# Performance work log

Measured on AMD Instinct MI355X. Metric: run time of the kernel, lower is better.

## Reference

```python
import jax, jax.numpy as jnp
import numpy as np

EMBED_DIM = 1024
NUM_HEADS = 16
HEAD_DIM = EMBED_DIM // NUM_HEADS
B, N = 4, 2048
EPS = 1e-5


def rotate_half(x):
    x2d = x.reshape(x.shape[:-1] + (-1, 2))
    x1, x2 = x2d[..., 0], x2d[..., 1]
    return jnp.stack([-x2, x1], axis=-1).reshape(x.shape)


def apply_rotary_emb(freqs, t):
    return t * freqs[0] + rotate_half(t) * freqs[1]


def setup_inputs() -> dict:
    key = jax.random.key(0)
    ks = jax.random.split(key, 12)
    d = EMBED_DIM
    inp = {
        "x": jax.random.normal(ks[0], (B, N, d), jnp.float32),
        "encoding": jax.random.normal(ks[1], (2, N, HEAD_DIM), jnp.float32),
        "Wqkv_w": jax.random.normal(ks[2], (d, 3 * d), jnp.float32) * (1.0 / np.sqrt(d)),
        "Wqkv_b": jnp.zeros((3 * d,), jnp.float32),
        "out_w": jax.random.normal(ks[3], (d, d), jnp.float32) * (1.0 / np.sqrt(d)),
        "out_b": jnp.zeros((d,), jnp.float32),
        "ffn0_w": jax.random.normal(ks[4], (2 * d, 2 * d), jnp.float32) * (1.0 / np.sqrt(2 * d)),
        "ffn0_b": jnp.zeros((2 * d,), jnp.float32),
        "ln_scale": jnp.ones((2 * d,), jnp.float32),
        "ln_bias": jnp.zeros((2 * d,), jnp.float32),
        "ffn3_w": jax.random.normal(ks[5], (2 * d, d), jnp.float32) * (1.0 / np.sqrt(2 * d)),
        "ffn3_b": jnp.zeros((d,), jnp.float32),
    }
    return inp


def reference(x, encoding, Wqkv_w, Wqkv_b, out_w, out_b, ffn0_w, ffn0_b, ln_scale, ln_bias, ffn3_w, ffn3_b):
    b, n, d = x.shape
    # fused QKV projection
    qkv = jnp.einsum('bnd,de->bne', x, Wqkv_w) + Wqkv_b
    qkv = qkv.reshape(b, n, NUM_HEADS, HEAD_DIM, 3).transpose(0, 2, 1, 3, 4)  # (b,h,n,hd,3)
    q, k, v = qkv[..., 0], qkv[..., 1], qkv[..., 2]
    # RoPE (encoding broadcasts over batch/heads)
    q = apply_rotary_emb(encoding, q)
    k = apply_rotary_emb(encoding, k)
    # attention (no mask)
    scale = 1.0 / jnp.sqrt(jnp.asarray(HEAD_DIM, x.dtype))
    logits = jnp.einsum('bhqd,bhkd->bhqk', q, k) * scale
    attn = jax.nn.softmax(logits, axis=-1)
    context = jnp.einsum('bhqk,bhkd->bhqd', attn, v)
    message = context.transpose(0, 2, 1, 3).reshape(b, n, d)
    message = jnp.einsum('bnd,de->bne', message, out_w) + out_b
    # FFN: concat -> Dense -> LayerNorm -> GELU(exact) -> Dense
    h = jnp.concatenate([x, message], axis=-1)
    h = jnp.einsum('bnd,de->bne', h, ffn0_w) + ffn0_b
    mu = jnp.mean(h, axis=-1, keepdims=True)
    var = jnp.mean(jnp.square(h - mu), axis=-1, keepdims=True)
    h = (h - mu) * jax.lax.rsqrt(var + EPS) * ln_scale + ln_bias
    h = jax.nn.gelu(h, approximate=False)
    res = jnp.einsum('bnd,de->bne', h, ffn3_w) + ffn3_b
    return x + res
```

## Files before the change

### kernel.cpp

```cpp
#include <hip/hip_runtime.h>
#include <hip/hip_bf16.h>
#include <math.h>

typedef __bf16 bf16x8 __attribute__((ext_vector_type(8)));
typedef float f32x4 __attribute__((ext_vector_type(4)));

#define MFMA16(a, b, c) __builtin_amdgcn_mfma_f32_16x16x32_bf16((a), (b), (c), 0, 0, 0)

__device__ __forceinline__ void gload16(const void* g, void* l) {
  __builtin_amdgcn_global_load_lds((const __attribute__((address_space(1))) void*)g,
                                   (__attribute__((address_space(3))) void*)l, 16, 0, 0);
}

__global__ __launch_bounds__(256) void transpose_bf16(const float* __restrict__ in,
                                                      __bf16* __restrict__ out,
                                                      int K, int Nn) {
  __shared__ float tile[32][33];
  int n0 = blockIdx.x * 32, k0 = blockIdx.y * 32;
  int tx = threadIdx.x & 31, ty = threadIdx.x >> 5;
#pragma unroll
  for (int r = 0; r < 32; r += 8)
    tile[ty + r][tx] = in[(size_t)(k0 + ty + r) * Nn + n0 + tx];
  __syncthreads();
#pragma unroll
  for (int r = 0; r < 32; r += 8)
    out[(size_t)(n0 + ty + r) * K + k0 + tx] = (__bf16)tile[tx][ty + r];
}

__global__ __launch_bounds__(256) void convert_x(const float* __restrict__ x,
                                                 __bf16* __restrict__ h) {
  int id = blockIdx.x * 256 + threadIdx.x;
  int row = id >> 7, cc = id & 127;
  const float* src = x + (size_t)row * 1024 + cc * 8;
  __bf16 tmp[8];
#pragma unroll
  for (int e = 0; e < 8; ++e) tmp[e] = (__bf16)src[e];
  *(uint4*)(h + (size_t)row * 2048 + cc * 8) = *(uint4*)tmp;
}

template <typename OutT, bool HAS_RES>
__global__ __launch_bounds__(256) void gemm_kernel(
    const __bf16* __restrict__ A, int lda,
    const __bf16* __restrict__ Bt,
    const float* __restrict__ bias,
    OutT* __restrict__ C, int ldc,
    const float* __restrict__ res,
    int M, int Nn, int K) {
  __shared__ __attribute__((aligned(16))) __bf16 As[128 * 64];
  __shared__ __attribute__((aligned(16))) __bf16 Bs[128 * 64];

  const int t = threadIdx.x;
  const int row0A = blockIdx.x * 128;
  const int row0B = blockIdx.y * 128;
  const int wave = t >> 6, lane = t & 63;
  const int wm = wave >> 1, wn = wave & 1;
  const int g = lane >> 4, lr = lane & 15;

  f32x4 acc[4][4] = {};

  for (int k0 = 0; k0 < K; k0 += 64) {
#pragma unroll
    for (int p = 0; p < 4; ++p) {
      int cbase = (wave * 4 + p) * 64;
      int ci = cbase + lane;
      int r = ci >> 3, cp = ci & 7, cl = cp ^ (r & 7);
      gload16(A + (size_t)(row0A + r) * lda + k0 + cl * 8, &As[cbase * 8]);
      gload16(Bt + (size_t)(row0B + r) * K + k0 + cl * 8, &Bs[cbase * 8]);
    }
    __syncthreads();
#pragma unroll
    for (int kk = 0; kk < 2; ++kk) {
      bf16x8 af[4], bfr[4];
#pragma unroll
      for (int mt = 0; mt < 4; ++mt) {
        int r = wm * 64 + mt * 16 + lr, c = kk * 4 + g;
        af[mt] = *(const bf16x8*)((char*)As + r * 128 + ((c ^ (r & 7)) * 16));
      }
#pragma unroll
      for (int nt = 0; nt < 4; ++nt) {
        int r = wn * 64 + nt * 16 + lr, c = kk * 4 + g;
        bfr[nt] = *(const bf16x8*)((char*)Bs + r * 128 + ((c ^ (r & 7)) * 16));
      }
#pragma unroll
      for (int mt = 0; mt < 4; ++mt)
#pragma unroll
        for (int nt = 0; nt < 4; ++nt)
          acc[mt][nt] = MFMA16(af[mt], bfr[nt], acc[mt][nt]);
    }
    __syncthreads();
  }

  float bias_v[4];
#pragma unroll
  for (int nt = 0; nt < 4; ++nt) bias_v[nt] = bias[row0B + wn * 64 + nt * 16 + lr];
#pragma unroll
  for (int mt = 0; mt < 4; ++mt) {
    int grow_base = row0A + wm * 64 + mt * 16 + g * 4;
#pragma unroll
    for (int nt = 0; nt < 4; ++nt) {
      int gcol = row0B + wn * 64 + nt * 16 + lr;
#pragma unroll
      for (int j = 0; j < 4; ++j) {
        int grow = grow_base + j;
        float v = acc[mt][nt][j] + bias_v[nt];
        if (HAS_RES) v += res[(size_t)grow * ldc + gcol];
        C[(size_t)grow * ldc + gcol] = (OutT)v;
      }
    }
  }
}

__global__ __launch_bounds__(256) void rope_scatter(
    const __bf16* __restrict__ qkv, const float* __restrict__ enc,
    __bf16* __restrict__ q, __bf16* __restrict__ kk, __bf16* __restrict__ vt) {
  int bh = blockIdx.y;
  int b = bh >> 4, h = bh & 15;
  int n0 = blockIdx.x * 64;
  int t = threadIdx.x;
#pragma unroll
  for (int i = 0; i < 8; ++i) {
    int id = t + i * 256;
    int nl = id >> 5, p = id & 31;
    int n = n0 + nl;
    int d0 = 2 * p, d1 = 2 * p + 1;
    size_t base = ((size_t)(b * 2048 + n)) * 3072 + (h * 64 + d0) * 3;
    float q0 = (float)qkv[base + 0], k0 = (float)qkv[base + 1];
    float q1 = (float)qkv[base + 3], k1 = (float)qkv[base + 4];
    const float* e0 = enc + (size_t)n * 64;
    const float* e1 = enc + (size_t)131072 + (size_t)n * 64;
    float f00 = e0[d0], f01 = e0[d1], f10 = e1[d0], f11 = e1[d1];
    float qo0 = q0 * f00 - q1 * f10;
    float qo1 = q1 * f01 + q0 * f11;
    float ko0 = k0 * f00 - k1 * f10;
    float ko1 = k1 * f01 + k0 * f11;
    size_t qb = ((size_t)bh * 2048 + n) * 64 + d0;
    q[qb] = (__bf16)(qo0 * 0.125f);
    q[qb + 1] = (__bf16)(qo1 * 0.125f);
    kk[qb] = (__bf16)ko0;
    kk[qb + 1] = (__bf16)ko1;
  }
#pragma unroll
  for (int i = 0; i < 2; ++i) {
    int id = t + i * 256;
    int hd = id >> 3, c = id & 7;
    __bf16 tmp[8];
#pragma unroll
    for (int e = 0; e < 8; ++e) {
      int kv = (c >> 2) * 32 + (e >> 2) * 16 + (c & 3) * 4 + (e & 3);
      int n = n0 + kv;
      tmp[e] = qkv[((size_t)(b * 2048 + n)) * 3072 + (h * 64 + hd) * 3 + 2];
    }
    *(uint4*)(vt + ((size_t)bh * 64 + hd) * 2048 + n0 + c * 8) = *(uint4*)tmp;
  }
}

__global__ __launch_bounds__(256) void attn_kernel(
    const __bf16* __restrict__ q, const __bf16* __restrict__ k,
    const __bf16* __restrict__ vt, __bf16* __restrict__ ctx) {
  __shared__ __attribute__((aligned(16))) __bf16 Ks[2][64 * 64];
  __shared__ __attribute__((aligned(16))) __bf16 Vs[2][64 * 64];

  const int bh = blockIdx.y, b = bh >> 4, h = bh & 15;
  const int q0 = blockIdx.x * 64;
  const int t = threadIdx.x, wave = t >> 6, lane = t & 63;
  const int g = lane >> 4, lr = lane & 15;
  const int qrow = q0 + wave * 16;

  const __bf16* kbase = k + (size_t)bh * 2048 * 64;
  const __bf16* vbase = vt + (size_t)bh * 64 * 2048;

  bf16x8 qf[2];
#pragma unroll
  for (int kc = 0; kc < 2; ++kc)
    qf[kc] = *(const bf16x8*)(q + ((size_t)bh * 2048 + qrow + lr) * 64 + kc * 32 + g * 8);

  f32x4 o[4] = {};
  float lsum = 0.f;

#define STAGE_ATTN(buf, kv0)                                                    \
  {                                                                             \
    _Pragma("unroll") for (int p = 0; p < 2; ++p) {                             \
      int cbase = wave * 128 + p * 64;                                          \
      int ci = cbase + lane;                                                    \
      int r = ci >> 3, cp = ci & 7, cl = cp ^ (r & 7);                          \
      gload16(kbase + (size_t)((kv0) + r) * 64 + cl * 8, &Ks[buf][cbase * 8]);  \
      gload16(vbase + (size_t)r * 2048 + (kv0) + cl * 8, &Vs[buf][cbase * 8]);  \
    }                                                                           \
  }

  STAGE_ATTN(0, 0);
  __syncthreads();
  int buf = 0;

  for (int kv0 = 0; kv0 < 2048; kv0 += 64) {
    if (kv0 + 64 < 2048) STAGE_ATTN(buf ^ 1, kv0 + 64);

    f32x4 s[4];
#pragma unroll
    for (int nt = 0; nt < 4; ++nt) {
      int r = nt * 16 + lr;
      bf16x8 kf0 = *(const bf16x8*)((char*)Ks[buf] + r * 128 + (((0 * 4 + g) ^ (r & 7)) * 16));
      bf16x8 kf1 = *(const bf16x8*)((char*)Ks[buf] + r * 128 + (((1 * 4 + g) ^ (r & 7)) * 16));
      f32x4 a = {};
      a = MFMA16(kf0, qf[0], a);
      a = MFMA16(kf1, qf[1], a);
      s[nt] = a;
    }

    float pvv[4][4];
#pragma unroll
    for (int nt = 0; nt < 4; ++nt)
#pragma unroll
      for (int j = 0; j < 4; ++j) {
        float e = __expf(s[nt][j]);
        pvv[nt][j] = e;
        lsum += e;
      }

#pragma unroll
    for (int t2 = 0; t2 < 2; ++t2) {
      bf16x8 pf;
#pragma unroll
      for (int e = 0; e < 8; ++e) pf[e] = (__bf16)pvv[2 * t2 + (e >> 2)][e & 3];
#pragma unroll
      for (int nt = 0; nt < 4; ++nt) {
        int r = nt * 16 + lr;
        bf16x8 vf = *(const bf16x8*)((char*)Vs[buf] + r * 128 + (((t2 * 4 + g) ^ (r & 7)) * 16));
        o[nt] = MFMA16(vf, pf, o[nt]);
      }
    }
    __syncthreads();
    buf ^= 1;
  }

  lsum += __shfl_xor(lsum, 16, 64);
  lsum += __shfl_xor(lsum, 32, 64);
  float inv = 1.f / lsum;

  size_t obase = ((size_t)(b * 2048 + qrow + lr)) * 1024 + h * 64;
#pragma unroll
  for (int nt = 0; nt < 4; ++nt) {
    __bf16 w4[4];
#pragma unroll
    for (int j = 0; j < 4; ++j) w4[j] = (__bf16)(o[nt][j] * inv);
    *(uint2*)(ctx + obase + nt * 16 + g * 4) = *(uint2*)w4;
  }
#undef STAGE_ATTN
}

__global__ __launch_bounds__(256) void ln_gelu(const __bf16* __restrict__ hin,
                                               const float* __restrict__ lns,
                                               const float* __restrict__ lnb,
                                               __bf16* __restrict__ hout) {
  int row = blockIdx.x;
  const __bf16* rp = hin + (size_t)row * 2048;
  int t = threadIdx.x;
  __bf16 tmp[8];
  *(uint4*)tmp = *(const uint4*)(rp + t * 8);
  float vals[8], s = 0.f, s2 = 0.f;
#pragma unroll
  for (int e = 0; e < 8; ++e) {
    float x = (float)tmp[e];
    vals[e] = x;
    s += x;
    s2 += x * x;
  }
#pragma unroll
  for (int m = 1; m < 64; m <<= 1) {
    s += __shfl_xor(s, m, 64);
    s2 += __shfl_xor(s2, m, 64);
  }
  __shared__ float red[8];
  int wave = t >> 6, lane = t & 63;
  if (lane == 0) { red[wave] = s; red[4 + wave] = s2; }
  __syncthreads();
  s = red[0] + red[1] + red[2] + red[3];
  s2 = red[4] + red[5] + red[6] + red[7];
  float mu = s * (1.f / 2048.f);
  float var = s2 * (1.f / 2048.f) - mu * mu;
  float rstd = rsqrtf(var + 1e-5f);
  __bf16 outv[8];
#pragma unroll
  for (int e = 0; e < 8; ++e) {
    int c = t * 8 + e;
    float xh = (vals[e] - mu) * rstd * lns[c] + lnb[c];
    float gg = 0.5f * xh * (1.f + erff(xh * 0.70710678118f));
    outv[e] = (__bf16)gg;
  }
  *(uint4*)(hout + (size_t)row * 2048 + t * 8) = *(uint4*)outv;
}

extern "C" void kernel_launch(void* const* d_in, const int* in_sizes, int n_in,
                              void* d_out, int out_size, void* d_ws, size_t ws_size,
                              hipStream_t stream) {
  const float* x = (const float*)d_in[0];
  const float* enc = (const float*)d_in[1];
  const float* wqkv = (const float*)d_in[2];
  const float* bqkv = (const float*)d_in[3];
  const float* wout = (const float*)d_in[4];
  const float* bout = (const float*)d_in[5];
  const float* wffn0 = (const float*)d_in[6];
  const float* bffn0 = (const float*)d_in[7];
  const float* lns = (const float*)d_in[8];
  const float* lnb = (const float*)d_in[9];
  const float* wffn3 = (const float*)d_in[10];
  const float* bffn3 = (const float*)d_in[11];
  float* out = (float*)d_out;
  char* ws = (char*)d_ws;

  __bf16* wT_qkv = (__bf16*)(ws + 0);
  __bf16* wT_out = (__bf16*)(ws + 6291456);
  __bf16* wT_ffn0 = (__bf16*)(ws + 8388608);
  __bf16* wT_ffn3 = (__bf16*)(ws + 16777216);
  __bf16* h_in = (__bf16*)(ws + 20971520);
  __bf16* qkv = (__bf16*)(ws + 54525952);
  __bf16* ffn0o = qkv;
  __bf16* qb = (__bf16*)(ws + 104857600);
  __bf16* h2 = qb;
  __bf16* kb = (__bf16*)(ws + 121634816);
  __bf16* vtb = (__bf16*)(ws + 138412032);
  __bf16* ctx = (__bf16*)(ws + 155189248);

  dim3 blk(256);
  transpose_bf16<<<dim3(96, 32), blk, 0, stream>>>(wqkv, wT_qkv, 1024, 3072);
  transpose_bf16<<<dim3(32, 32), blk, 0, stream>>>(wout, wT_out, 1024, 1024);
  transpose_bf16<<<dim3(64, 64), blk, 0, stream>>>(wffn0, wT_ffn0, 2048, 2048);
  transpose_bf16<<<dim3(32, 64), blk, 0, stream>>>(wffn3, wT_ffn3, 2048, 1024);
  convert_x<<<4096, blk, 0, stream>>>(x, h_in);

  gemm_kernel<__bf16, false><<<dim3(64, 24), blk, 0, stream>>>(
      h_in, 2048, wT_qkv, bqkv, qkv, 3072, nullptr, 8192, 3072, 1024);

  rope_scatter<<<dim3(32, 64), blk, 0, stream>>>(qkv, enc, qb, kb, vtb);
  attn_kernel<<<dim3(32, 64), blk, 0, stream>>>(qb, kb, vtb, ctx);

  gemm_kernel<__bf16, false><<<dim3(64, 8), blk, 0, stream>>>(
      ctx, 1024, wT_out, bout, h_in + 1024, 2048, nullptr, 8192, 1024, 1024);

  gemm_kernel<__bf16, false><<<dim3(64, 16), blk, 0, stream>>>(
      h_in, 2048, wT_ffn0, bffn0, ffn0o, 2048, nullptr, 8192, 2048, 2048);

  ln_gelu<<<8192, blk, 0, stream>>>(ffn0o, lns, lnb, h2);

  gemm_kernel<float, true><<<dim3(64, 8), blk, 0, stream>>>(
      h2, 2048, wT_ffn3, bffn3, out, 1024, x, 8192, 1024, 2048);
}
```

Baseline: 422.9 us.

## Fold out-projection into FFN0 weights, add 256-tile pipelined GEMM, permute QKV layout

The out-projection weight is folded algebraically into the second half of the FFN0 weight, and its bias into the FFN0 bias. This removes the separate out-projection GEMM, and attention writes its context straight into the concat buffer. The QKV weight columns are permuted so that q, k and v come out contiguous, which lets the RoPE/scatter kernel use vectorized loads. A new 256x256 tile GEMM with a 4-stage global_load_lds pipeline, split barriers and setprio runs the QKV and FFN0 projections, and setprio hints are added around the attention MFMAs. The weight folding is recomputed every call, adding small prologue work, and it adds one more bf16 rounding step on the fused weights.

After: 467.1 us. 1.1x slower.

```diff
diff --git a/kernel.cpp b/kernel.cpp
--- a/kernel.cpp
+++ b/kernel.cpp
@@ -6,6 +6,7 @@
 typedef float f32x4 __attribute__((ext_vector_type(4)));
 
 #define MFMA16(a, b, c) __builtin_amdgcn_mfma_f32_16x16x32_bf16((a), (b), (c), 0, 0, 0)
+#define KAP(r) ((((r) + ((r) >> 2))) & 3)
 
 __device__ __forceinline__ void gload16(const void* g, void* l) {
   __builtin_amdgcn_global_load_lds((const __attribute__((address_space(1))) void*)g,
@@ -27,6 +28,43 @@
     out[(size_t)(n0 + ty + r) * K + k0 + tx] = (__bf16)tile[tx][ty + r];
 }
 
+__global__ __launch_bounds__(256) void transpose_qkv_perm(const float* __restrict__ in,
+                                                          __bf16* __restrict__ out) {
+  __shared__ float tile[32][33];
+  int n0 = blockIdx.x * 32, k0 = blockIdx.y * 32;
+  int tx = threadIdx.x & 31, ty = threadIdx.x >> 5;
+#pragma unroll
+  for (int r = 0; r < 32; r += 8)
+    tile[ty + r][tx] = in[(size_t)(k0 + ty + r) * 3072 + n0 + tx];
+  __syncthreads();
+#pragma unroll
+  for (int r = 0; r < 32; r += 8) {
+    int n = n0 + ty + r;
+    int h = n / 192, rem = n % 192, hd = rem / 3, which = rem % 3;
+    int np = which * 1024 + h * 64 + hd;
+    out[(size_t)np * 1024 + k0 + tx] = (__bf16)tile[tx][ty + r];
+  }
+}
+
+__global__ __launch_bounds__(256) void bias_perm(const float* __restrict__ b,
+                                                 float* __restrict__ bp) {
+  int n = blockIdx.x * 256 + threadIdx.x;
+  if (n < 3072) {
+    int h = n / 192, rem = n % 192, hd = rem / 3, which = rem % 3;
+    bp[which * 1024 + h * 64 + hd] = b[n];
+  }
+}
+
+__global__ __launch_bounds__(256) void convert_plain(const float* __restrict__ in,
+                                                     __bf16* __restrict__ out) {
+  int id = blockIdx.x * 256 + threadIdx.x;
+  const float* src = in + (size_t)id * 8;
+  __bf16 tmp[8];
+#pragma unroll
+  for (int e = 0; e < 8; ++e) tmp[e] = (__bf16)src[e];
+  *(uint4*)(out + (size_t)id * 8) = *(uint4*)tmp;
+}
+
 __global__ __launch_bounds__(256) void convert_x(const float* __restrict__ x,
                                                  __bf16* __restrict__ h) {
   int id = blockIdx.x * 256 + threadIdx.x;
@@ -38,7 +76,25 @@
   *(uint4*)(h + (size_t)row * 2048 + cc * 8) = *(uint4*)tmp;
 }
 
-template <typename OutT, bool HAS_RES>
+__global__ __launch_bounds__(256) void copy_cols(const __bf16* __restrict__ src,
+                                                 __bf16* __restrict__ dst) {
+  int id = blockIdx.x * 256 + threadIdx.x;
+  int row = id >> 7, c = id & 127;
+  *(uint4*)(dst + (size_t)row * 2048 + 1024 + c * 8) =
+      *(const uint4*)(src + (size_t)row * 1024 + c * 8);
+}
+
+__global__ __launch_bounds__(256) void fuse_bias(const float* __restrict__ bout,
+                                                 const float* __restrict__ w0,
+                                                 const float* __restrict__ b0,
+                                                 float* __restrict__ bf) {
+  int n = blockIdx.x * 256 + threadIdx.x;
+  float s = b0[n];
+  for (int e = 0; e < 1024; ++e) s += bout[e] * w0[(size_t)(1024 + e) * 2048 + n];
+  bf[n] = s;
+}
+
+template <typename OutT, bool HAS_RES, bool HAS_BIAS>
 __global__ __launch_bounds__(256) void gemm_kernel(
     const __bf16* __restrict__ A, int lda,
     const __bf16* __restrict__ Bt,
@@ -92,7 +148,8 @@
 
   float bias_v[4];
 #pragma unroll
-  for (int nt = 0; nt < 4; ++nt) bias_v[nt] = bias[row0B + wn * 64 + nt * 16 + lr];
+  for (int nt = 0; nt < 4; ++nt)
+    bias_v[nt] = HAS_BIAS ? bias[row0B + wn * 64 + nt * 16 + lr] : 0.f;
 #pragma unroll
   for (int mt = 0; mt < 4; ++mt) {
     int grow_base = row0A + wm * 64 + mt * 16 + g * 4;
@@ -106,6 +163,115 @@
         if (HAS_RES) v += res[(size_t)grow * ldc + gcol];
         C[(size_t)grow * ldc + gcol] = (OutT)v;
       }
+    }
+  }
+}
+
+template <typename OutT>
+__global__ __launch_bounds__(512, 2) void gemm256(
+    const __bf16* __restrict__ A, int lda,
+    const __bf16* __restrict__ Bt, int ldb,
+    const float* __restrict__ bias,
+    OutT* __restrict__ C, int ldc, int K) {
+  __shared__ __attribute__((aligned(16))) __bf16 lds[65536];
+  __bf16* Asl = lds;
+  __bf16* Bsl = lds + 32768;
+
+  const int t = threadIdx.x;
+  const int wave = t >> 6, lane = t & 63;
+  const int wm = wave >> 2, wn = wave & 3;
+  const int g = lane >> 4, lr = lane & 15;
+  const int row0A = blockIdx.x * 256, row0B = blockIdx.y * 256;
+
+  f32x4 acc[8][4] = {};
+  const int L = K >> 5;
+
+#define STAGE_A(s)                                                           \
+  {                                                                          \
+    int ssl = (s) & 3;                                                       \
+    _Pragma("unroll") for (int l = 0; l < 2; ++l) {                          \
+      int cbase = (wave * 2 + l) * 64;                                       \
+      int ci = cbase + lane, r = ci >> 2, c = (ci & 3) ^ KAP(r);             \
+      gload16(A + (size_t)(row0A + r) * lda + (s) * 32 + c * 8,              \
+              (void*)(Asl + ssl * 8192 + cbase * 8));                        \
+    }                                                                        \
+  }
+#define STAGE_B(s)                                                           \
+  {                                                                          \
+    int ssl = (s) & 3;                                                       \
+    _Pragma("unroll") for (int l = 0; l < 2; ++l) {                          \
+      int cbase = (wave * 2 + l) * 64;                                       \
+      int ci = cbase + lane, r = ci >> 2, c = (ci & 3) ^ KAP(r);             \
+      gload16(Bt + (size_t)(row0B + r) * ldb + (s) * 32 + c * 8,             \
+              (void*)(Bsl + ssl * 8192 + cbase * 8));                        \
+    }                                                                        \
+  }
+
+#define SLOT_BODY(s, DO_STAGE, VMSTR)                                        \
+  {                                                                          \
+    const __bf16* Ab = Asl + ((s) & 3) * 8192;                               \
+    const __bf16* Bb = Bsl + ((s) & 3) * 8192;                               \
+    bf16x8 bfrag[4], afrag[4];                                               \
+    _Pragma("unroll") for (int ni = 0; ni < 4; ++ni) {                       \
+      int rr = wn * 64 + ni * 16 + lr;                                       \
+      bfrag[ni] = *(const bf16x8*)(Bb + rr * 32 + ((g ^ KAP(rr)) * 8));      \
+    }                                                                        \
+    _Pragma("unroll") for (int mi = 0; mi < 4; ++mi) {                       \
+      int rr = wm * 128 + mi * 16 + lr;                                      \
+      afrag[mi] = *(const bf16x8*)(Ab + rr * 32 + ((g ^ KAP(rr)) * 8));      \
+    }                                                                        \
+    if (DO_STAGE) STAGE_A((s) + 3);                                          \
+    __builtin_amdgcn_s_barrier();                                            \
+    __builtin_amdgcn_s_setprio(1);                                           \
+    _Pragma("unroll") for (int mi = 0; mi < 4; ++mi)                         \
+      _Pragma("unroll") for (int ni = 0; ni < 4; ++ni)                       \
+        acc[mi][ni] = MFMA16(afrag[mi], bfrag[ni], acc[mi][ni]);             \
+    __builtin_amdgcn_s_setprio(0);                                           \
+    __builtin_amdgcn_s_barrier();                                            \
+    _Pragma("unroll") for (int mi = 0; mi < 4; ++mi) {                       \
+      int rr = wm * 128 + 64 + mi * 16 + lr;                                 \
+      afrag[mi] = *(const bf16x8*)(Ab + rr * 32 + ((g ^ KAP(rr)) * 8));      \
+    }                                                                        \
+    if (DO_STAGE) STAGE_B((s) + 3);                                          \
+    asm volatile("s_waitcnt " VMSTR ::: "memory");                           \
+    __builtin_amdgcn_s_barrier();                                            \
+    __builtin_amdgcn_s_setprio(1);                                           \
+    _Pragma("unroll") for (int mi = 0; mi < 4; ++mi)                         \
+      _Pragma("unroll") for (int ni = 0; ni < 4; ++ni)                       \
+        acc[4 + mi][ni] = MFMA16(afrag[mi], bfrag[ni], acc[4 + mi][ni]);     \
+    __builtin_amdgcn_s_setprio(0);                                           \
+    __builtin_amdgcn_s_barrier();                                            \
+  }
+
+#pragma unroll
+  for (int ss = 0; ss < 3; ++ss) {
+    STAGE_A(ss);
+    STAGE_B(ss);
+  }
+  asm volatile("s_waitcnt vmcnt(8)" ::: "memory");
+  __builtin_amdgcn_s_barrier();
+
+  for (int s = 0; s + 3 < L; ++s) SLOT_BODY(s, true, "vmcnt(8)");
+  SLOT_BODY(L - 3, false, "vmcnt(4)");
+  SLOT_BODY(L - 2, false, "vmcnt(0)");
+  SLOT_BODY(L - 1, false, "vmcnt(0)");
+
+#undef SLOT_BODY
+#undef STAGE_A
+#undef STAGE_B
+
+  float bias_v[4];
+#pragma unroll
+  for (int ni = 0; ni < 4; ++ni) bias_v[ni] = bias[row0B + wn * 64 + ni * 16 + lr];
+#pragma unroll
+  for (int mi = 0; mi < 8; ++mi) {
+    int grow_base = row0A + wm * 128 + mi * 16 + g * 4;
+#pragma unroll
+    for (int ni = 0; ni < 4; ++ni) {
+      int gcol = row0B + wn * 64 + ni * 16 + lr;
+#pragma unroll
+      for (int j = 0; j < 4; ++j)
+        C[(size_t)(grow_base + j) * ldc + gcol] = (OutT)(acc[mi][ni][j] + bias_v[ni]);
     }
   }
 }
@@ -118,26 +284,29 @@
   int n0 = blockIdx.x * 64;
   int t = threadIdx.x;
 #pragma unroll
-  for (int i = 0; i < 8; ++i) {
+  for (int i = 0; i < 2; ++i) {
     int id = t + i * 256;
-    int nl = id >> 5, p = id & 31;
+    int nl = id >> 3, cc = id & 7;
     int n = n0 + nl;
-    int d0 = 2 * p, d1 = 2 * p + 1;
-    size_t base = ((size_t)(b * 2048 + n)) * 3072 + (h * 64 + d0) * 3;
-    float q0 = (float)qkv[base + 0], k0 = (float)qkv[base + 1];
-    float q1 = (float)qkv[base + 3], k1 = (float)qkv[base + 4];
-    const float* e0 = enc + (size_t)n * 64;
-    const float* e1 = enc + (size_t)131072 + (size_t)n * 64;
-    float f00 = e0[d0], f01 = e0[d1], f10 = e1[d0], f11 = e1[d1];
-    float qo0 = q0 * f00 - q1 * f10;
-    float qo1 = q1 * f01 + q0 * f11;
-    float ko0 = k0 * f00 - k1 * f10;
-    float ko1 = k1 * f01 + k0 * f11;
-    size_t qb = ((size_t)bh * 2048 + n) * 64 + d0;
-    q[qb] = (__bf16)(qo0 * 0.125f);
-    q[qb + 1] = (__bf16)(qo1 * 0.125f);
-    kk[qb] = (__bf16)ko0;
-    kk[qb + 1] = (__bf16)ko1;
+    size_t row = (size_t)(b * 2048 + n) * 3072;
+    bf16x8 qv = *(const bf16x8*)(qkv + row + h * 64 + cc * 8);
+    bf16x8 kv = *(const bf16x8*)(qkv + row + 1024 + h * 64 + cc * 8);
+    const float* e0 = enc + (size_t)n * 64 + cc * 8;
+    const float* e1 = e0 + 131072;
+    __bf16 qo[8], ko[8];
+#pragma unroll
+    for (int e = 0; e < 8; e += 2) {
+      float q0 = (float)qv[e], q1 = (float)qv[e + 1];
+      float k0 = (float)kv[e], k1 = (float)kv[e + 1];
+      float f00 = e0[e], f01 = e0[e + 1], f10 = e1[e], f11 = e1[e + 1];
+      qo[e] = (__bf16)((q0 * f00 - q1 * f10) * 0.125f);
+      qo[e + 1] = (__bf16)((q1 * f01 + q0 * f11) * 0.125f);
+      ko[e] = (__bf16)(k0 * f00 - k1 * f10);
+      ko[e + 1] = (__bf16)(k1 * f01 + k0 * f11);
+    }
+    size_t qb = ((size_t)bh * 2048 + n) * 64 + cc * 8;
+    *(uint4*)(q + qb) = *(uint4*)qo;
+    *(uint4*)(kk + qb) = *(uint4*)ko;
   }
 #pragma unroll
   for (int i = 0; i < 2; ++i) {
@@ -148,7 +317,7 @@
     for (int e = 0; e < 8; ++e) {
       int kv = (c >> 2) * 32 + (e >> 2) * 16 + (c & 3) * 4 + (e & 3);
       int n = n0 + kv;
-      tmp[e] = qkv[((size_t)(b * 2048 + n)) * 3072 + (h * 64 + hd) * 3 + 2];
+      tmp[e] = qkv[(size_t)(b * 2048 + n) * 3072 + 2048 + h * 64 + hd];
     }
     *(uint4*)(vt + ((size_t)bh * 64 + hd) * 2048 + n0 + c * 8) = *(uint4*)tmp;
   }
@@ -196,16 +365,18 @@
     if (kv0 + 64 < 2048) STAGE_ATTN(buf ^ 1, kv0 + 64);
 
     f32x4 s[4];
+    __builtin_amdgcn_s_setprio(1);
 #pragma unroll
     for (int nt = 0; nt < 4; ++nt) {
       int r = nt * 16 + lr;
-      bf16x8 kf0 = *(const bf16x8*)((char*)Ks[buf] + r * 128 + (((0 * 4 + g) ^ (r & 7)) * 16));
-      bf16x8 kf1 = *(const bf16x8*)((char*)Ks[buf] + r * 128 + (((1 * 4 + g) ^ (r & 7)) * 16));
+      bf16x8 kf0 = *(const bf16x8*)((char*)Ks[buf] + r * 128 + ((g ^ (r & 7)) * 16));
+      bf16x8 kf1 = *(const bf16x8*)((char*)Ks[buf] + r * 128 + (((4 + g) ^ (r & 7)) * 16));
       f32x4 a = {};
       a = MFMA16(kf0, qf[0], a);
       a = MFMA16(kf1, qf[1], a);
       s[nt] = a;
     }
+    __builtin_amdgcn_s_setprio(0);
 
     float pvv[4][4];
 #pragma unroll
@@ -217,6 +388,7 @@
         lsum += e;
       }
 
+    __builtin_amdgcn_s_setprio(1);
 #pragma unroll
     for (int t2 = 0; t2 < 2; ++t2) {
       bf16x8 pf;
@@ -229,6 +401,7 @@
         o[nt] = MFMA16(vf, pf, o[nt]);
       }
     }
+    __builtin_amdgcn_s_setprio(0);
     __syncthreads();
     buf ^= 1;
   }
@@ -237,7 +410,7 @@
   lsum += __shfl_xor(lsum, 32, 64);
   float inv = 1.f / lsum;
 
-  size_t obase = ((size_t)(b * 2048 + qrow + lr)) * 1024 + h * 64;
+  size_t obase = ((size_t)(b * 2048 + qrow + lr)) * 2048 + 1024 + h * 64;
 #pragma unroll
   for (int nt = 0; nt < 4; ++nt) {
     __bf16 w4[4];
@@ -309,39 +482,43 @@
   char* ws = (char*)d_ws;
 
   __bf16* wT_qkv = (__bf16*)(ws + 0);
-  __bf16* wT_out = (__bf16*)(ws + 6291456);
-  __bf16* wT_ffn0 = (__bf16*)(ws + 8388608);
-  __bf16* wT_ffn3 = (__bf16*)(ws + 16777216);
-  __bf16* h_in = (__bf16*)(ws + 20971520);
-  __bf16* qkv = (__bf16*)(ws + 54525952);
+  __bf16* wT_ffn0 = (__bf16*)(ws + 6291456);
+  __bf16* wT_ffn3 = (__bf16*)(ws + 14680064);
+  __bf16* wout_bf = (__bf16*)(ws + 18874368);
+  __bf16* wpT_tmp = (__bf16*)(ws + 20971520);
+  float* bqkv_p = (float*)(ws + 25165824);
+  float* bffn0_f = (float*)(ws + 25178112);
+  __bf16* h_in = (__bf16*)(ws + 25186304);
+  __bf16* qkv = (__bf16*)(ws + 58740736);
   __bf16* ffn0o = qkv;
-  __bf16* qb = (__bf16*)(ws + 104857600);
+  __bf16* qb = (__bf16*)(ws + 109072384);
   __bf16* h2 = qb;
-  __bf16* kb = (__bf16*)(ws + 121634816);
-  __bf16* vtb = (__bf16*)(ws + 138412032);
-  __bf16* ctx = (__bf16*)(ws + 155189248);
+  __bf16* kb = (__bf16*)(ws + 125849600);
+  __bf16* vtb = (__bf16*)(ws + 142626816);
 
   dim3 blk(256);
-  transpose_bf16<<<dim3(96, 32), blk, 0, stream>>>(wqkv, wT_qkv, 1024, 3072);
-  transpose_bf16<<<dim3(32, 32), blk, 0, stream>>>(wout, wT_out, 1024, 1024);
+  transpose_qkv_perm<<<dim3(96, 32), blk, 0, stream>>>(wqkv, wT_qkv);
+  bias_perm<<<12, blk, 0, stream>>>(bqkv, bqkv_p);
   transpose_bf16<<<dim3(64, 64), blk, 0, stream>>>(wffn0, wT_ffn0, 2048, 2048);
   transpose_bf16<<<dim3(32, 64), blk, 0, stream>>>(wffn3, wT_ffn3, 2048, 1024);
+  convert_plain<<<512, blk, 0, stream>>>(wout, wout_bf);
+  gemm_kernel<__bf16, false, false><<<dim3(16, 8), blk, 0, stream>>>(
+      wT_ffn0 + 1024, 2048, wout_bf, nullptr, wpT_tmp, 1024, nullptr, 2048, 1024, 1024);
+  copy_cols<<<1024, blk, 0, stream>>>(wpT_tmp, wT_ffn0);
+  fuse_bias<<<8, blk, 0, stream>>>(bout, wffn0, bffn0, bffn0_f);
   convert_x<<<4096, blk, 0, stream>>>(x, h_in);
 
-  gemm_kernel<__bf16, false><<<dim3(64, 24), blk, 0, stream>>>(
-      h_in, 2048, wT_qkv, bqkv, qkv, 3072, nullptr, 8192, 3072, 1024);
+  gemm256<__bf16><<<dim3(32, 12), dim3(512), 0, stream>>>(
+      h_in, 2048, wT_qkv, 1024, bqkv_p, qkv, 3072, 1024);
 
   rope_scatter<<<dim3(32, 64), blk, 0, stream>>>(qkv, enc, qb, kb, vtb);
-  attn_kernel<<<dim3(32, 64), blk, 0, stream>>>(qb, kb, vtb, ctx);
-
-  gemm_kernel<__bf16, false><<<dim3(64, 8), blk, 0, stream>>>(
-      ctx, 1024, wT_out, bout, h_in + 1024, 2048, nullptr, 8192, 1024, 1024);
-
-  gemm_kernel<__bf16, false><<<dim3(64, 16), blk, 0, stream>>>(
-      h_in, 2048, wT_ffn0, bffn0, ffn0o, 2048, nullptr, 8192, 2048, 2048);
+  attn_kernel<<<dim3(32, 64), blk, 0, stream>>>(qb, kb, vtb, h_in);
+
+  gemm256<__bf16><<<dim3(32, 8), dim3(512), 0, stream>>>(
+      h_in, 2048, wT_ffn0, 2048, bffn0_f, ffn0o, 2048, 2048);
 
   ln_gelu<<<8192, blk, 0, stream>>>(ffn0o, lns, lnb, h2);
 
-  gemm_kernel<float, true><<<dim3(64, 8), blk, 0, stream>>>(
+  gemm_kernel<float, true, true><<<dim3(64, 8), blk, 0, stream>>>(
       h2, 2048, wT_ffn3, bffn3, out, 1024, x, 8192, 1024, 2048);
 }
```
